# Performance work log

Measured on AMD Instinct MI355X. Metric: run time of the kernel, lower is better.

The kernel has to match this reference:

```python
import jax, jax.numpy as jnp
import numpy as np

D_MODEL = 1024
NUM_HEADS = 16
HEAD_DIM = D_MODEL // NUM_HEADS
SEQ_LEN = 2048
THETA = 10000.0


def setup_inputs() -> dict:
    key = jax.random.key(0)
    ks = jax.random.split(key, 9)
    s = 1.0 / np.sqrt(D_MODEL)
    inp = {
        "x": jax.random.normal(ks[0], (2, SEQ_LEN, D_MODEL), dtype=jnp.float32),
        "Wq": jax.random.uniform(ks[1], (D_MODEL, D_MODEL), jnp.float32, -s, s),
        "bq": jax.random.uniform(ks[2], (D_MODEL,), jnp.float32, -s, s),
        "Wk": jax.random.uniform(ks[3], (D_MODEL, D_MODEL), jnp.float32, -s, s),
        "bk": jax.random.uniform(ks[4], (D_MODEL,), jnp.float32, -s, s),
        "Wv": jax.random.uniform(ks[5], (D_MODEL, D_MODEL), jnp.float32, -s, s),
        "bv": jax.random.uniform(ks[6], (D_MODEL,), jnp.float32, -s, s),
        "Wo": jax.random.uniform(ks[7], (D_MODEL, D_MODEL), jnp.float32, -s, s),
        "bo": jax.random.uniform(ks[8], (D_MODEL,), jnp.float32, -s, s),
    }
    return inp


def _rope_cos_sin(seq_len, dim, theta):
    inv_freq = 1.0 / theta ** (jnp.arange(0, dim, 2, dtype=jnp.float32) / dim)  # [dim/2]
    t = jnp.arange(seq_len, dtype=jnp.float32)
    freqs = jnp.outer(t, inv_freq)  # [S, dim/2]
    return jnp.cos(freqs), jnp.sin(freqs)


def _apply_rope(x, cos, sin):
    # x: [B, H, S, head_dim]; interleaved complex pairs (even, odd)
    x2 = x.reshape(*x.shape[:-1], -1, 2)  # [B,H,S,hd/2,2]
    xe, xo = x2[..., 0], x2[..., 1]
    c = cos[None, None, :, :]
    s = sin[None, None, :, :]
    oe = xe * c - xo * s
    oo = xe * s + xo * c
    return jnp.stack([oe, oo], axis=-1).reshape(x.shape)


def reference(x, Wq, bq, Wk, bk, Wv, bv, Wo, bo):
    B, S, D = x.shape
    H, hd = NUM_HEADS, HEAD_DIM
    q = x @ Wq.T + bq
    k = x @ Wk.T + bk
    v = x @ Wv.T + bv
    # [B, H, S, hd]
    q = q.reshape(B, S, H, hd).transpose(0, 2, 1, 3)
    k = k.reshape(B, S, H, hd).transpose(0, 2, 1, 3)
    v = v.reshape(B, S, H, hd).transpose(0, 2, 1, 3)
    cos, sin = _rope_cos_sin(S, hd, THETA)
    q = _apply_rope(q, cos, sin)
    k = _apply_rope(k, cos, sin)
    scores = jnp.einsum("bhqd,bhkd->bhqk", q, k) / jnp.sqrt(jnp.float32(hd))
    causal = jnp.triu(jnp.ones((S, S), dtype=bool), k=1)
    scores = jnp.where(causal[None, None, :, :], -jnp.inf, scores)
    attn = jax.nn.softmax(scores, axis=-1)
    out = jnp.einsum("bhqk,bhkd->bhqd", attn, v)
    out = out.transpose(0, 2, 1, 3).reshape(B, S, D)
    return out @ Wo.T + bo
```

## Files before the change

kernel.cpp:

```cpp
#include <hip/hip_runtime.h>
#include <hip/hip_bf16.h>

#define S_LEN 2048
#define DM 1024
#define NH 16
#define HD 64
#define M_ROWS 4096
#define LOG2E 1.4426950408889634f

typedef __attribute__((ext_vector_type(8))) short short8;
typedef __attribute__((ext_vector_type(4))) float f32x4;
typedef __attribute__((ext_vector_type(16))) float f32x16;

__device__ inline ushort f2b(float f) {
  union { float f; unsigned u; } v; v.f = f;
  unsigned r = v.u + 0x7fffu + ((v.u >> 16) & 1u);
  return (ushort)(r >> 16);
}

__device__ inline unsigned pk_bf16(float a, float b) {
  __hip_bfloat162 h = __float22bfloat162_rn(make_float2(a, b));
  union { __hip_bfloat162 h; unsigned u; } v; v.h = h;
  return v.u;
}

__device__ inline float fexp2(float x) { return __builtin_amdgcn_exp2f(x); }

__device__ inline void gl_lds16(const void* g, void* l) {
  __builtin_amdgcn_global_load_lds(
      (const __attribute__((address_space(1))) void*)g,
      (__attribute__((address_space(3))) void*)l, 16, 0, 0);
}

__global__ __launch_bounds__(256) void cast_all_kernel(
    const float* __restrict__ x, const float* __restrict__ Wq, const float* __restrict__ Wk,
    const float* __restrict__ Wv, const float* __restrict__ Wo,
    ushort* __restrict__ xb, ushort* __restrict__ Wqb, ushort* __restrict__ Wkb,
    ushort* __restrict__ Wvb, ushort* __restrict__ Wob) {
  int i = blockIdx.x * 256 + threadIdx.x;
  int r = i >> 18, off = i & 0x3FFFF;
  const float4* s;
  uint2* d;
  switch (r) {
    case 0: case 1: case 2: case 3: s = (const float4*)x + i;  d = (uint2*)xb + i;  break;
    case 4: s = (const float4*)Wq + off; d = (uint2*)Wqb + off; break;
    case 5: s = (const float4*)Wk + off; d = (uint2*)Wkb + off; break;
    case 6: s = (const float4*)Wv + off; d = (uint2*)Wvb + off; break;
    default: s = (const float4*)Wo + off; d = (uint2*)Wob + off; break;
  }
  float4 v = *s;
  uint2 o;
  o.x = pk_bf16(v.x, v.y);
  o.y = pk_bf16(v.z, v.w);
  *d = o;
}

__global__ __launch_bounds__(256) void rope_table_kernel(float* __restrict__ C, float* __restrict__ Sn) {
  int idx = blockIdx.x * blockDim.x + threadIdx.x;
  int s = idx >> 5, i = idx & 31;
  float inv = exp2f(-(float)i * (13.287712379549449f / 32.0f));
  float a = (float)s * inv;
  C[idx] = cosf(a);
  Sn[idx] = sinf(a);
}

__device__ inline void gemm128_mainloop(const ushort* __restrict__ A, const ushort* __restrict__ W,
                                        int m0, int n0, f32x4 acc[4][4],
                                        ushort* As, ushort* Bs) {
  const int t = threadIdx.x, lane = t & 63, wave = t >> 6;
  const int wr = (wave >> 1) * 64, wc = (wave & 1) * 64;
  const int lr = lane & 15, lg = lane >> 4;
  const int slot0 = wave * 128 + lane, slot1 = slot0 + 64;
  const int row0 = slot0 >> 2, g0 = (slot0 & 3) ^ (row0 & 3);
  const int row1 = slot1 >> 2, g1 = (slot1 & 3) ^ (row1 & 3);
  const int lo0 = wave * 128 * 8, lo1 = lo0 + 64 * 8;

#pragma unroll
  for (int a = 0; a < 4; a++)
#pragma unroll
    for (int b = 0; b < 4; b++) acc[a][b] = (f32x4){0.f, 0.f, 0.f, 0.f};

  for (int k0 = 0; k0 < DM; k0 += 32) {
    __syncthreads();
    gl_lds16(&A[(size_t)(m0 + row0) * DM + k0 + g0 * 8], &As[lo0]);
    gl_lds16(&A[(size_t)(m0 + row1) * DM + k0 + g1 * 8], &As[lo1]);
    gl_lds16(&W[(size_t)(n0 + row0) * DM + k0 + g0 * 8], &Bs[lo0]);
    gl_lds16(&W[(size_t)(n0 + row1) * DM + k0 + g1 * 8], &Bs[lo1]);
    __syncthreads();
    short8 af[4], bf[4];
#pragma unroll
    for (int mt = 0; mt < 4; mt++)
      af[mt] = *(const short8*)&As[((wr + mt * 16 + lr) * 4 + (lg ^ (lr & 3))) * 8];
#pragma unroll
    for (int nt = 0; nt < 4; nt++)
      bf[nt] = *(const short8*)&Bs[((wc + nt * 16 + lr) * 4 + (lg ^ (lr & 3))) * 8];
#pragma unroll
    for (int mt = 0; mt < 4; mt++)
#pragma unroll
      for (int nt = 0; nt < 4; nt++)
        acc[mt][nt] = __builtin_amdgcn_mfma_f32_16x16x32_bf16(af[mt], bf[nt], acc[mt][nt], 0, 0, 0);
  }
}

__global__ __launch_bounds__(256) void gemm_qkv_kernel(const ushort* __restrict__ xb,
    const ushort* __restrict__ Wqb, const ushort* __restrict__ Wkb, const ushort* __restrict__ Wvb,
    const float* __restrict__ bq, const float* __restrict__ bk, const float* __restrict__ bv,
    const float* __restrict__ ropeC, const float* __restrict__ ropeS,
    ushort* __restrict__ qb, ushort* __restrict__ kb, ushort* __restrict__ vT) {
  __shared__ ushort As[4096];
  __shared__ ushort Bs[4096];
  const int z = blockIdx.z;
  const ushort* W = (z == 0) ? Wqb : ((z == 1) ? Wkb : Wvb);
  const float* bias = (z == 0) ? bq : ((z == 1) ? bk : bv);
  const int m0 = blockIdx.x * 128, n0 = blockIdx.y * 128;
  f32x4 acc[4][4];
  gemm128_mainloop(xb, W, m0, n0, acc, As, Bs);

  const int t = threadIdx.x, lane = t & 63, wave = t >> 6;
  const int wr = (wave >> 1) * 64, wc = (wave & 1) * 64;
  const int lr = lane & 15, lg = lane >> 4;
  const bool evenlane = (lane & 1) == 0;

#pragma unroll
  for (int mt = 0; mt < 4; mt++) {
#pragma unroll
    for (int nt = 0; nt < 4; nt++) {
      const int n = n0 + wc + nt * 16 + lr;
      const float bn = bias[n];
      const int h = n >> 6, d = n & 63, i = (n & 63) >> 1;
#pragma unroll
      for (int r = 0; r < 4; r++) {
        const int m = m0 + wr + mt * 16 + lg * 4 + r;
        const int s = m & (S_LEN - 1);
        const int b = m >> 11;
        float v = acc[mt][nt][r] + bn;
        if (z < 2) {
          float c = ropeC[s * 32 + i];
          float sn = ropeS[s * 32 + i];
          float w = __shfl_xor(v, 1);
          v = v * c + (evenlane ? -w * sn : w * sn);
          if (z == 0) v *= 0.125f;
          ushort* dst = (z == 0) ? qb : kb;
          dst[(((size_t)b * NH + h) * S_LEN + s) * HD + d] = f2b(v);
        } else {
          vT[(((size_t)b * NH + h) * HD + d) * S_LEN + s] = f2b(v);
        }
      }
    }
  }
}

__global__ __launch_bounds__(256) void flash_kernel(const ushort* __restrict__ qb,
                                                    const ushort* __restrict__ kb,
                                                    const ushort* __restrict__ vT,
                                                    ushort* __restrict__ attn_out) {
  __shared__ ushort Ks[2][4096];
  __shared__ ushort VTs[2][4096];
  const int t = threadIdx.x, lane = t & 63, wave = t >> 6;
  const int q31 = lane & 31, h = lane >> 5;
  const int y = blockIdx.y;
  const int qt = (y & 16) ? (int)blockIdx.x : (15 - (int)blockIdx.x);
  const int q0 = qt * 128;
  const int nkt = 2 * qt + 2;
  const ushort* kbh = kb + (size_t)y * S_LEN * HD;
  const ushort* vbh = vT + (size_t)y * HD * S_LEN;

  const int qrow = q0 + wave * 32 + q31;
  const ushort* qptr = qb + ((size_t)y * S_LEN + qrow) * HD + h * 8;
  short8 qf[4];
#pragma unroll
  for (int s = 0; s < 4; s++) qf[s] = *(const short8*)(qptr + s * 16);

  const int slot0 = wave * 128 + lane, slot1 = slot0 + 64;
  const int row0 = slot0 >> 3, g0 = (slot0 & 7) ^ (row0 & 7);
  const int row1 = slot1 >> 3, g1 = (slot1 & 7) ^ (row1 & 7);
  const int lo0 = wave * 128 * 8, lo1 = lo0 + 64 * 8;

  gl_lds16(kbh + (size_t)row0 * HD + g0 * 8, &Ks[0][lo0]);
  gl_lds16(kbh + (size_t)row1 * HD + g1 * 8, &Ks[0][lo1]);
  gl_lds16(vbh + (size_t)row0 * S_LEN + g0 * 8, &VTs[0][lo0]);
  gl_lds16(vbh + (size_t)row1 * S_LEN + g1 * 8, &VTs[0][lo1]);
  __syncthreads();

  f32x16 O[2];
#pragma unroll
  for (int st = 0; st < 2; st++)
#pragma unroll
    for (int r = 0; r < 16; r++) O[st][r] = 0.f;
  float m_i = -1e30f, l_i = 0.f;
  int cur = 0;

  for (int kt = 0; kt < nkt; kt++) {
    if (kt + 1 < nkt) {
      const int k0n = (kt + 1) * 64;
      gl_lds16(kbh + (size_t)(k0n + row0) * HD + g0 * 8, &Ks[cur ^ 1][lo0]);
      gl_lds16(kbh + (size_t)(k0n + row1) * HD + g1 * 8, &Ks[cur ^ 1][lo1]);
      gl_lds16(vbh + (size_t)row0 * S_LEN + k0n + g0 * 8, &VTs[cur ^ 1][lo0]);
      gl_lds16(vbh + (size_t)row1 * S_LEN + k0n + g1 * 8, &VTs[cur ^ 1][lo1]);
    }
    const ushort* Kb = Ks[cur];
    const ushort* Vb = VTs[cur];

    f32x16 sc[2];
#pragma unroll
    for (int st = 0; st < 2; st++)
#pragma unroll
      for (int r = 0; r < 16; r++) sc[st][r] = 0.f;
#pragma unroll
    for (int s = 0; s < 4; s++) {
#pragma unroll
      for (int st = 0; st < 2; st++) {
        const int row = st * 32 + q31;
        const short8 kf = *(const short8*)&Kb[(row * 8 + ((2 * s + h) ^ (row & 7))) * 8];
        sc[st] = __builtin_amdgcn_mfma_f32_32x32x16_bf16(kf, qf[s], sc[st], 0, 0, 0);
      }
    }
    if (kt * 64 + 63 > q0 + wave * 32) {
#pragma unroll
      for (int st = 0; st < 2; st++)
#pragma unroll
        for (int r = 0; r < 16; r++) {
          const int kcol = kt * 64 + st * 32 + (r & 3) + 8 * (r >> 2) + 4 * h;
          if (kcol > qrow) sc[st][r] = -1e30f;
        }
    }
    float mx = sc[0][0];
#pragma unroll
    for (int st = 0; st < 2; st++)
#pragma unroll
      for (int r = 0; r < 16; r++) mx = fmaxf(mx, sc[st][r]);
    mx = fmaxf(mx, __shfl_xor(mx, 32));
    const float mnew = fmaxf(m_i, mx);
    const float alpha = fexp2((m_i - mnew) * LOG2E);
    const float nmw = -mnew * LOG2E;
    float su = 0.f;
#pragma unroll
    for (int st = 0; st < 2; st++)
#pragma unroll
      for (int r = 0; r < 16; r++) {
        const float p = fexp2(fmaf(sc[st][r], LOG2E, nmw));
        sc[st][r] = p;
        su += p;
      }
    su += __shfl_xor(su, 32);
    l_i = l_i * alpha + su;
    m_i = mnew;
#pragma unroll
    for (int st = 0; st < 2; st++)
#pragma unroll
      for (int r = 0; r < 16; r++) O[st][r] *= alpha;

    unsigned pp[8][2];
#pragma unroll
    for (int st = 0; st < 2; st++)
#pragma unroll
      for (int rg = 0; rg < 4; rg++) {
        pp[st * 4 + rg][0] = pk_bf16(sc[st][4 * rg + 0], sc[st][4 * rg + 1]);
        pp[st * 4 + rg][1] = pk_bf16(sc[st][4 * rg + 2], sc[st][4 * rg + 3]);
      }
#pragma unroll
    for (int s = 0; s < 4; s++) {
      const unsigned sA0 = pp[2 * s][0], sA1 = pp[2 * s][1];
      const unsigned sB0 = pp[2 * s + 1][0], sB1 = pp[2 * s + 1][1];
      const unsigned send0 = h ? sA0 : sB0;
      const unsigned send1 = h ? sA1 : sB1;
      const unsigned recv0 = (unsigned)__shfl_xor((int)send0, 32);
      const unsigned recv1 = (unsigned)__shfl_xor((int)send1, 32);
      unsigned bfr[4];
      bfr[0] = h ? recv0 : sA0;
      bfr[1] = h ? recv1 : sA1;
      bfr[2] = h ? sB0 : recv0;
      bfr[3] = h ? sB1 : recv1;
      union { unsigned u[4]; short8 v; } pf;
      pf.u[0] = bfr[0]; pf.u[1] = bfr[1]; pf.u[2] = bfr[2]; pf.u[3] = bfr[3];
#pragma unroll
      for (int st = 0; st < 2; st++) {
        const int row = st * 32 + q31;
        const short8 vf = *(const short8*)&Vb[(row * 8 + ((2 * s + h) ^ (row & 7))) * 8];
        O[st] = __builtin_amdgcn_mfma_f32_32x32x16_bf16(vf, pf.v, O[st], 0, 0, 0);
      }
    }
    __syncthreads();
    cur ^= 1;
  }

  const int b = y >> 4, hh = y & 15;
  const float linv = 1.f / l_i;
  ushort* arow = attn_out + ((size_t)b * S_LEN + qrow) * DM + hh * HD;
#pragma unroll
  for (int st = 0; st < 2; st++)
#pragma unroll
    for (int rg = 0; rg < 4; rg++) {
      const int d0 = st * 32 + 8 * rg + 4 * h;
      *(unsigned*)&arow[d0] = pk_bf16(O[st][4 * rg + 0] * linv, O[st][4 * rg + 1] * linv);
      *(unsigned*)&arow[d0 + 2] = pk_bf16(O[st][4 * rg + 2] * linv, O[st][4 * rg + 3] * linv);
    }
}

__global__ __launch_bounds__(256) void gemm_out_kernel(const ushort* __restrict__ attn,
                                                       const ushort* __restrict__ Wob,
                                                       const float* __restrict__ bo,
                                                       float* __restrict__ out) {
  __shared__ ushort As[4096];
  __shared__ ushort Bs[4096];
  const int m0 = blockIdx.x * 128, n0 = blockIdx.y * 128;
  f32x4 acc[4][4];
  gemm128_mainloop(attn, Wob, m0, n0, acc, As, Bs);

  const int t = threadIdx.x, lane = t & 63, wave = t >> 6;
  const int wr = (wave >> 1) * 64, wc = (wave & 1) * 64;
  const int lr = lane & 15, lg = lane >> 4;
#pragma unroll
  for (int mt = 0; mt < 4; mt++) {
#pragma unroll
    for (int nt = 0; nt < 4; nt++) {
      const int n = n0 + wc + nt * 16 + lr;
      const float bn = bo[n];
#pragma unroll
      for (int r = 0; r < 4; r++) {
        const int m = m0 + wr + mt * 16 + lg * 4 + r;
        out[(size_t)m * DM + n] = acc[mt][nt][r] + bn;
      }
    }
  }
}

extern "C" void kernel_launch(void* const* d_in, const int* in_sizes, int n_in,
                              void* d_out, int out_size, void* d_ws, size_t ws_size,
                              hipStream_t stream) {
  const float* x  = (const float*)d_in[0];
  const float* Wq = (const float*)d_in[1];
  const float* bq = (const float*)d_in[2];
  const float* Wk = (const float*)d_in[3];
  const float* bk = (const float*)d_in[4];
  const float* Wv = (const float*)d_in[5];
  const float* bv = (const float*)d_in[6];
  const float* Wo = (const float*)d_in[7];
  const float* bo = (const float*)d_in[8];
  float* out = (float*)d_out;

  char* ws = (char*)d_ws;
  size_t off = 0;
  auto alloc = [&](size_t bytes) { char* p = ws + off; off += (bytes + 255) & ~255ull; return p; };
  ushort* xb   = (ushort*)alloc((size_t)M_ROWS * DM * 2);
  ushort* Wqb  = (ushort*)alloc((size_t)DM * DM * 2);
  ushort* Wkb  = (ushort*)alloc((size_t)DM * DM * 2);
  ushort* Wvb  = (ushort*)alloc((size_t)DM * DM * 2);
  ushort* Wob  = (ushort*)alloc((size_t)DM * DM * 2);
  ushort* qb   = (ushort*)alloc((size_t)M_ROWS * DM * 2);
  ushort* kb   = (ushort*)alloc((size_t)M_ROWS * DM * 2);
  ushort* vTb  = (ushort*)alloc((size_t)M_ROWS * DM * 2);
  ushort* attn = (ushort*)alloc((size_t)M_ROWS * DM * 2);
  float* ropeC = (float*)alloc((size_t)S_LEN * 32 * 4);
  float* ropeS = (float*)alloc((size_t)S_LEN * 32 * 4);
  (void)ws_size; (void)in_sizes; (void)n_in; (void)out_size;

  cast_all_kernel<<<8192, 256, 0, stream>>>(x, Wq, Wk, Wv, Wo, xb, Wqb, Wkb, Wvb, Wob);
  rope_table_kernel<<<(S_LEN * 32) / 256, 256, 0, stream>>>(ropeC, ropeS);
  gemm_qkv_kernel<<<dim3(M_ROWS / 128, DM / 128, 3), 256, 0, stream>>>(
      xb, Wqb, Wkb, Wvb, bq, bk, bv, ropeC, ropeS, qb, kb, vTb);
  flash_kernel<<<dim3(16, 2 * NH), 256, 0, stream>>>(qb, kb, vTb, attn);
  gemm_out_kernel<<<dim3(M_ROWS / 128, DM / 128), 256, 0, stream>>>(attn, Wob, bo, out);
}
```

Baseline: 215.4 us.

## Split flash attention across KV halves, restage QKV epilogue, retile output GEMM

Flash attention now splits each (batch, head) KV range into even and odd 64-key tiles, processed by separate blocks. This doubles the grid. A new combine kernel merges the two partial outputs using their per-row max and sum. The QKV GEMM moves to a 64-wide K step and stages its output tile through LDS, so RoPE is applied in a vectorized pass and Q, K and V^T are written with coalesced 16-byte stores. The output GEMM uses 128x64 tiles to launch more blocks. The cost is an extra kernel launch, a round trip of partial outputs through memory, and a finite mask value that must stay harmless for fully masked half-tiles.

```diff
diff --git a/kernel.cpp b/kernel.cpp
--- a/kernel.cpp
+++ b/kernel.cpp
@@ -7,6 +7,7 @@
 #define HD 64
 #define M_ROWS 4096
 #define LOG2E 1.4426950408889634f
+#define MASKVAL -1.0e4f
 
 typedef __attribute__((ext_vector_type(8))) short short8;
 typedef __attribute__((ext_vector_type(4))) float f32x4;
@@ -16,6 +17,10 @@
   union { float f; unsigned u; } v; v.f = f;
   unsigned r = v.u + 0x7fffu + ((v.u >> 16) & 1u);
   return (ushort)(r >> 16);
+}
+
+__device__ inline float b2f(ushort u) {
+  union { unsigned u; float f; } v; v.u = ((unsigned)u) << 16; return v.f;
 }
 
 __device__ inline unsigned pk_bf16(float a, float b) {
@@ -64,88 +69,128 @@
   Sn[idx] = sinf(a);
 }
 
-__device__ inline void gemm128_mainloop(const ushort* __restrict__ A, const ushort* __restrict__ W,
-                                        int m0, int n0, f32x4 acc[4][4],
-                                        ushort* As, ushort* Bs) {
-  const int t = threadIdx.x, lane = t & 63, wave = t >> 6;
-  const int wr = (wave >> 1) * 64, wc = (wave & 1) * 64;
-  const int lr = lane & 15, lg = lane >> 4;
-  const int slot0 = wave * 128 + lane, slot1 = slot0 + 64;
-  const int row0 = slot0 >> 2, g0 = (slot0 & 3) ^ (row0 & 3);
-  const int row1 = slot1 >> 2, g1 = (slot1 & 3) ^ (row1 & 3);
-  const int lo0 = wave * 128 * 8, lo1 = lo0 + 64 * 8;
-
-#pragma unroll
-  for (int a = 0; a < 4; a++)
-#pragma unroll
-    for (int b = 0; b < 4; b++) acc[a][b] = (f32x4){0.f, 0.f, 0.f, 0.f};
-
-  for (int k0 = 0; k0 < DM; k0 += 32) {
-    __syncthreads();
-    gl_lds16(&A[(size_t)(m0 + row0) * DM + k0 + g0 * 8], &As[lo0]);
-    gl_lds16(&A[(size_t)(m0 + row1) * DM + k0 + g1 * 8], &As[lo1]);
-    gl_lds16(&W[(size_t)(n0 + row0) * DM + k0 + g0 * 8], &Bs[lo0]);
-    gl_lds16(&W[(size_t)(n0 + row1) * DM + k0 + g1 * 8], &Bs[lo1]);
-    __syncthreads();
-    short8 af[4], bf[4];
-#pragma unroll
-    for (int mt = 0; mt < 4; mt++)
-      af[mt] = *(const short8*)&As[((wr + mt * 16 + lr) * 4 + (lg ^ (lr & 3))) * 8];
-#pragma unroll
-    for (int nt = 0; nt < 4; nt++)
-      bf[nt] = *(const short8*)&Bs[((wc + nt * 16 + lr) * 4 + (lg ^ (lr & 3))) * 8];
-#pragma unroll
-    for (int mt = 0; mt < 4; mt++)
-#pragma unroll
-      for (int nt = 0; nt < 4; nt++)
-        acc[mt][nt] = __builtin_amdgcn_mfma_f32_16x16x32_bf16(af[mt], bf[nt], acc[mt][nt], 0, 0, 0);
-  }
-}
-
 __global__ __launch_bounds__(256) void gemm_qkv_kernel(const ushort* __restrict__ xb,
     const ushort* __restrict__ Wqb, const ushort* __restrict__ Wkb, const ushort* __restrict__ Wvb,
     const float* __restrict__ bq, const float* __restrict__ bk, const float* __restrict__ bv,
     const float* __restrict__ ropeC, const float* __restrict__ ropeS,
     ushort* __restrict__ qb, ushort* __restrict__ kb, ushort* __restrict__ vT) {
-  __shared__ ushort As[4096];
-  __shared__ ushort Bs[4096];
+  __shared__ ushort lds[128 * 136];
+  ushort* As = lds;
+  ushort* Bs = lds + 8192;
   const int z = blockIdx.z;
   const ushort* W = (z == 0) ? Wqb : ((z == 1) ? Wkb : Wvb);
   const float* bias = (z == 0) ? bq : ((z == 1) ? bk : bv);
   const int m0 = blockIdx.x * 128, n0 = blockIdx.y * 128;
-  f32x4 acc[4][4];
-  gemm128_mainloop(xb, W, m0, n0, acc, As, Bs);
-
   const int t = threadIdx.x, lane = t & 63, wave = t >> 6;
   const int wr = (wave >> 1) * 64, wc = (wave & 1) * 64;
   const int lr = lane & 15, lg = lane >> 4;
-  const bool evenlane = (lane & 1) == 0;
-
+
+  int rows_[4], gs_[4], slots_[4];
+#pragma unroll
+  for (int j = 0; j < 4; j++) {
+    const int slot = wave * 256 + j * 64 + lane;
+    slots_[j] = slot;
+    rows_[j] = slot >> 3;
+    gs_[j] = (slot & 7) ^ (rows_[j] & 7);
+  }
+
+  f32x4 acc[4][4];
+#pragma unroll
+  for (int a = 0; a < 4; a++)
+#pragma unroll
+    for (int b = 0; b < 4; b++) acc[a][b] = (f32x4){0.f, 0.f, 0.f, 0.f};
+
+  for (int k0 = 0; k0 < DM; k0 += 64) {
+    __syncthreads();
+#pragma unroll
+    for (int j = 0; j < 4; j++)
+      gl_lds16(&xb[(size_t)(m0 + rows_[j]) * DM + k0 + gs_[j] * 8], &As[slots_[j] * 8]);
+#pragma unroll
+    for (int j = 0; j < 4; j++)
+      gl_lds16(&W[(size_t)(n0 + rows_[j]) * DM + k0 + gs_[j] * 8], &Bs[slots_[j] * 8]);
+    __syncthreads();
+#pragma unroll
+    for (int s32 = 0; s32 < 2; s32++) {
+      short8 af[4], bf[4];
+#pragma unroll
+      for (int mt = 0; mt < 4; mt++) {
+        const int row = wr + mt * 16 + lr;
+        af[mt] = *(const short8*)&As[(row * 8 + ((s32 * 4 + lg) ^ (row & 7))) * 8];
+      }
+#pragma unroll
+      for (int nt = 0; nt < 4; nt++) {
+        const int row = wc + nt * 16 + lr;
+        bf[nt] = *(const short8*)&Bs[(row * 8 + ((s32 * 4 + lg) ^ (row & 7))) * 8];
+      }
+#pragma unroll
+      for (int mt = 0; mt < 4; mt++)
+#pragma unroll
+        for (int nt = 0; nt < 4; nt++)
+          acc[mt][nt] = __builtin_amdgcn_mfma_f32_16x16x32_bf16(af[mt], bf[nt], acc[mt][nt], 0, 0, 0);
+    }
+  }
+
+  __syncthreads();
 #pragma unroll
   for (int mt = 0; mt < 4; mt++) {
 #pragma unroll
     for (int nt = 0; nt < 4; nt++) {
-      const int n = n0 + wc + nt * 16 + lr;
-      const float bn = bias[n];
-      const int h = n >> 6, d = n & 63, i = (n & 63) >> 1;
+      const int nloc = wc + nt * 16 + lr;
+      const float bn = bias[n0 + nloc];
 #pragma unroll
       for (int r = 0; r < 4; r++) {
-        const int m = m0 + wr + mt * 16 + lg * 4 + r;
-        const int s = m & (S_LEN - 1);
-        const int b = m >> 11;
-        float v = acc[mt][nt][r] + bn;
-        if (z < 2) {
-          float c = ropeC[s * 32 + i];
-          float sn = ropeS[s * 32 + i];
-          float w = __shfl_xor(v, 1);
-          v = v * c + (evenlane ? -w * sn : w * sn);
-          if (z == 0) v *= 0.125f;
-          ushort* dst = (z == 0) ? qb : kb;
-          dst[(((size_t)b * NH + h) * S_LEN + s) * HD + d] = f2b(v);
-        } else {
-          vT[(((size_t)b * NH + h) * HD + d) * S_LEN + s] = f2b(v);
-        }
-      }
+        const int mloc = wr + mt * 16 + lg * 4 + r;
+        const ushort v = f2b(acc[mt][nt][r] + bn);
+        if (z < 2) lds[mloc * 136 + nloc] = v;
+        else       lds[nloc * 136 + mloc] = v;
+      }
+    }
+  }
+  __syncthreads();
+
+  const int b = m0 >> 11;
+  if (z < 2) {
+    ushort* dst = (z == 0) ? qb : kb;
+    const float qscale = (z == 0) ? 0.125f : 1.0f;
+#pragma unroll
+    for (int c = 0; c < 8; c++) {
+      const int sloc = c * 16 + (t >> 4);
+      const int nloc = (t & 15) * 8;
+      short8 val = *(const short8*)&lds[sloc * 136 + nloc];
+      const int s = (m0 + sloc) & (S_LEN - 1);
+      const int h = (n0 + nloc) >> 6;
+      const int d0 = nloc & 63;
+      const float4 cv = *(const float4*)&ropeC[s * 32 + d0 / 2];
+      const float4 sv = *(const float4*)&ropeS[s * 32 + d0 / 2];
+      uint4 o;
+      {
+        float e = b2f((ushort)val[0]), od = b2f((ushort)val[1]);
+        o.x = pk_bf16((e * cv.x - od * sv.x) * qscale, (e * sv.x + od * cv.x) * qscale);
+      }
+      {
+        float e = b2f((ushort)val[2]), od = b2f((ushort)val[3]);
+        o.y = pk_bf16((e * cv.y - od * sv.y) * qscale, (e * sv.y + od * cv.y) * qscale);
+      }
+      {
+        float e = b2f((ushort)val[4]), od = b2f((ushort)val[5]);
+        o.z = pk_bf16((e * cv.z - od * sv.z) * qscale, (e * sv.z + od * cv.z) * qscale);
+      }
+      {
+        float e = b2f((ushort)val[6]), od = b2f((ushort)val[7]);
+        o.w = pk_bf16((e * cv.w - od * sv.w) * qscale, (e * sv.w + od * cv.w) * qscale);
+      }
+      *(uint4*)&dst[(((size_t)b * NH + h) * S_LEN + s) * HD + d0] = o;
+    }
+  } else {
+    const int sbase = m0 & (S_LEN - 1);
+#pragma unroll
+    for (int c = 0; c < 8; c++) {
+      const int nloc = c * 16 + (t >> 4);
+      const int s0 = (t & 15) * 8;
+      short8 val = *(const short8*)&lds[nloc * 136 + s0];
+      const int h = (n0 + nloc) >> 6;
+      const int d = nloc & 63;
+      *(short8*)&vT[(((size_t)b * NH + h) * HD + d) * S_LEN + sbase + s0] = val;
     }
   }
 }
@@ -153,20 +198,21 @@
 __global__ __launch_bounds__(256) void flash_kernel(const ushort* __restrict__ qb,
                                                     const ushort* __restrict__ kb,
                                                     const ushort* __restrict__ vT,
-                                                    ushort* __restrict__ attn_out) {
+                                                    ushort* __restrict__ Oh,
+                                                    float2* __restrict__ ml) {
   __shared__ ushort Ks[2][4096];
   __shared__ ushort VTs[2][4096];
   const int t = threadIdx.x, lane = t & 63, wave = t >> 6;
   const int q31 = lane & 31, h = lane >> 5;
   const int y = blockIdx.y;
+  const int bh = y >> 1, half = y & 1;
   const int qt = (y & 16) ? (int)blockIdx.x : (15 - (int)blockIdx.x);
   const int q0 = qt * 128;
-  const int nkt = 2 * qt + 2;
-  const ushort* kbh = kb + (size_t)y * S_LEN * HD;
-  const ushort* vbh = vT + (size_t)y * HD * S_LEN;
+  const ushort* kbh = kb + (size_t)bh * S_LEN * HD;
+  const ushort* vbh = vT + (size_t)bh * HD * S_LEN;
 
   const int qrow = q0 + wave * 32 + q31;
-  const ushort* qptr = qb + ((size_t)y * S_LEN + qrow) * HD + h * 8;
+  const ushort* qptr = qb + ((size_t)bh * S_LEN + qrow) * HD + h * 8;
   short8 qf[4];
 #pragma unroll
   for (int s = 0; s < 4; s++) qf[s] = *(const short8*)(qptr + s * 16);
@@ -176,10 +222,13 @@
   const int row1 = slot1 >> 3, g1 = (slot1 & 7) ^ (row1 & 7);
   const int lo0 = wave * 128 * 8, lo1 = lo0 + 64 * 8;
 
-  gl_lds16(kbh + (size_t)row0 * HD + g0 * 8, &Ks[0][lo0]);
-  gl_lds16(kbh + (size_t)row1 * HD + g1 * 8, &Ks[0][lo1]);
-  gl_lds16(vbh + (size_t)row0 * S_LEN + g0 * 8, &VTs[0][lo0]);
-  gl_lds16(vbh + (size_t)row1 * S_LEN + g1 * 8, &VTs[0][lo1]);
+  {
+    const int k00 = half * 64;
+    gl_lds16(kbh + (size_t)(k00 + row0) * HD + g0 * 8, &Ks[0][lo0]);
+    gl_lds16(kbh + (size_t)(k00 + row1) * HD + g1 * 8, &Ks[0][lo1]);
+    gl_lds16(vbh + (size_t)row0 * S_LEN + k00 + g0 * 8, &VTs[0][lo0]);
+    gl_lds16(vbh + (size_t)row1 * S_LEN + k00 + g1 * 8, &VTs[0][lo1]);
+  }
   __syncthreads();
 
   f32x16 O[2];
@@ -187,12 +236,13 @@
   for (int st = 0; st < 2; st++)
 #pragma unroll
     for (int r = 0; r < 16; r++) O[st][r] = 0.f;
-  float m_i = -1e30f, l_i = 0.f;
+  float m_i = MASKVAL, l_i = 0.f;
   int cur = 0;
 
-  for (int kt = 0; kt < nkt; kt++) {
-    if (kt + 1 < nkt) {
-      const int k0n = (kt + 1) * 64;
+  for (int idx = 0; idx <= qt; idx++) {
+    const int kt = half + 2 * idx;
+    if (idx < qt) {
+      const int k0n = (kt + 2) * 64;
       gl_lds16(kbh + (size_t)(k0n + row0) * HD + g0 * 8, &Ks[cur ^ 1][lo0]);
       gl_lds16(kbh + (size_t)(k0n + row1) * HD + g1 * 8, &Ks[cur ^ 1][lo1]);
       gl_lds16(vbh + (size_t)row0 * S_LEN + k0n + g0 * 8, &VTs[cur ^ 1][lo0]);
@@ -221,7 +271,7 @@
 #pragma unroll
         for (int r = 0; r < 16; r++) {
           const int kcol = kt * 64 + st * 32 + (r & 3) + 8 * (r >> 2) + 4 * h;
-          if (kcol > qrow) sc[st][r] = -1e30f;
+          if (kcol > qrow) sc[st][r] = MASKVAL;
         }
     }
     float mx = sc[0][0];
@@ -266,13 +316,11 @@
       const unsigned send1 = h ? sA1 : sB1;
       const unsigned recv0 = (unsigned)__shfl_xor((int)send0, 32);
       const unsigned recv1 = (unsigned)__shfl_xor((int)send1, 32);
-      unsigned bfr[4];
-      bfr[0] = h ? recv0 : sA0;
-      bfr[1] = h ? recv1 : sA1;
-      bfr[2] = h ? sB0 : recv0;
-      bfr[3] = h ? sB1 : recv1;
       union { unsigned u[4]; short8 v; } pf;
-      pf.u[0] = bfr[0]; pf.u[1] = bfr[1]; pf.u[2] = bfr[2]; pf.u[3] = bfr[3];
+      pf.u[0] = h ? recv0 : sA0;
+      pf.u[1] = h ? recv1 : sA1;
+      pf.u[2] = h ? sB0 : recv0;
+      pf.u[3] = h ? sB1 : recv1;
 #pragma unroll
       for (int st = 0; st < 2; st++) {
         const int row = st * 32 + q31;
@@ -284,17 +332,47 @@
     cur ^= 1;
   }
 
-  const int b = y >> 4, hh = y & 15;
-  const float linv = 1.f / l_i;
-  ushort* arow = attn_out + ((size_t)b * S_LEN + qrow) * DM + hh * HD;
+  ushort* obase = Oh + (((size_t)half * 32 + bh) * S_LEN + qrow) * HD;
 #pragma unroll
   for (int st = 0; st < 2; st++)
 #pragma unroll
     for (int rg = 0; rg < 4; rg++) {
       const int d0 = st * 32 + 8 * rg + 4 * h;
-      *(unsigned*)&arow[d0] = pk_bf16(O[st][4 * rg + 0] * linv, O[st][4 * rg + 1] * linv);
-      *(unsigned*)&arow[d0 + 2] = pk_bf16(O[st][4 * rg + 2] * linv, O[st][4 * rg + 3] * linv);
-    }
+      uint2 w;
+      w.x = pk_bf16(O[st][4 * rg + 0], O[st][4 * rg + 1]);
+      w.y = pk_bf16(O[st][4 * rg + 2], O[st][4 * rg + 3]);
+      *(uint2*)&obase[d0] = w;
+    }
+  if (h == 0) ml[((size_t)half * 32 + bh) * S_LEN + qrow] = make_float2(m_i, l_i);
+}
+
+__global__ __launch_bounds__(256) void combine_kernel(const ushort* __restrict__ Oh,
+                                                      const float2* __restrict__ ml,
+                                                      ushort* __restrict__ attn) {
+  const int tid = blockIdx.x * 256 + threadIdx.x;
+  const int d8 = tid & 7;
+  const int q = (tid >> 3) & (S_LEN - 1);
+  const int bh = tid >> 14;
+  const float2 ml0 = ml[(size_t)bh * S_LEN + q];
+  const float2 ml1 = ml[((size_t)32 + bh) * S_LEN + q];
+  const float m = fmaxf(ml0.x, ml1.x);
+  const float w0 = fexp2((ml0.x - m) * LOG2E);
+  const float w1 = fexp2((ml1.x - m) * LOG2E);
+  const float inv = 1.f / (ml0.y * w0 + ml1.y * w1);
+  const uint4 a = *(const uint4*)&Oh[((size_t)bh * S_LEN + q) * HD + d8 * 8];
+  const uint4 bb = *(const uint4*)&Oh[(((size_t)32 + bh) * S_LEN + q) * HD + d8 * 8];
+  const unsigned au[4] = {a.x, a.y, a.z, a.w};
+  const unsigned bu[4] = {bb.x, bb.y, bb.z, bb.w};
+  uint4 o;
+  unsigned* op = (unsigned*)&o;
+#pragma unroll
+  for (int j = 0; j < 4; j++) {
+    const float a0 = b2f((ushort)(au[j] & 0xffff)), a1 = b2f((ushort)(au[j] >> 16));
+    const float b0 = b2f((ushort)(bu[j] & 0xffff)), b1 = b2f((ushort)(bu[j] >> 16));
+    op[j] = pk_bf16((a0 * w0 + b0 * w1) * inv, (a1 * w0 + b1 * w1) * inv);
+  }
+  const int b = bh >> 4, hh = bh & 15;
+  *(uint4*)&attn[((size_t)b * S_LEN + q) * DM + hh * HD + d8 * 8] = o;
 }
 
 __global__ __launch_bounds__(256) void gemm_out_kernel(const ushort* __restrict__ attn,
@@ -302,23 +380,56 @@
                                                        const float* __restrict__ bo,
                                                        float* __restrict__ out) {
   __shared__ ushort As[4096];
-  __shared__ ushort Bs[4096];
-  const int m0 = blockIdx.x * 128, n0 = blockIdx.y * 128;
-  f32x4 acc[4][4];
-  gemm128_mainloop(attn, Wob, m0, n0, acc, As, Bs);
-
+  __shared__ ushort Bs[2048];
+  const int m0 = blockIdx.x * 128, n0 = blockIdx.y * 64;
   const int t = threadIdx.x, lane = t & 63, wave = t >> 6;
-  const int wr = (wave >> 1) * 64, wc = (wave & 1) * 64;
+  const int wm = (wave >> 1) * 64, wn = (wave & 1) * 32;
   const int lr = lane & 15, lg = lane >> 4;
+  const int slotA0 = wave * 128 + lane, slotA1 = slotA0 + 64;
+  const int rowA0 = slotA0 >> 2, gA0 = (slotA0 & 3) ^ (rowA0 & 3);
+  const int rowA1 = slotA1 >> 2, gA1 = (slotA1 & 3) ^ (rowA1 & 3);
+  const int slotB = wave * 64 + lane;
+  const int rowB = slotB >> 2, gB = (slotB & 3) ^ (rowB & 3);
+
+  f32x4 acc[4][2];
+#pragma unroll
+  for (int a = 0; a < 4; a++)
+#pragma unroll
+    for (int b = 0; b < 2; b++) acc[a][b] = (f32x4){0.f, 0.f, 0.f, 0.f};
+
+  for (int k0 = 0; k0 < DM; k0 += 32) {
+    __syncthreads();
+    gl_lds16(&attn[(size_t)(m0 + rowA0) * DM + k0 + gA0 * 8], &As[slotA0 * 8]);
+    gl_lds16(&attn[(size_t)(m0 + rowA1) * DM + k0 + gA1 * 8], &As[slotA1 * 8]);
+    gl_lds16(&Wob[(size_t)(n0 + rowB) * DM + k0 + gB * 8], &Bs[slotB * 8]);
+    __syncthreads();
+    short8 af[4], bf[2];
+#pragma unroll
+    for (int mt = 0; mt < 4; mt++) {
+      const int row = wm + mt * 16 + lr;
+      af[mt] = *(const short8*)&As[(row * 4 + (lg ^ (row & 3))) * 8];
+    }
+#pragma unroll
+    for (int nt = 0; nt < 2; nt++) {
+      const int row = wn + nt * 16 + lr;
+      bf[nt] = *(const short8*)&Bs[(row * 4 + (lg ^ (row & 3))) * 8];
+    }
+#pragma unroll
+    for (int mt = 0; mt < 4; mt++)
+#pragma unroll
+      for (int nt = 0; nt < 2; nt++)
+        acc[mt][nt] = __builtin_amdgcn_mfma_f32_16x16x32_bf16(af[mt], bf[nt], acc[mt][nt], 0, 0, 0);
+  }
+
 #pragma unroll
   for (int mt = 0; mt < 4; mt++) {
 #pragma unroll
-    for (int nt = 0; nt < 4; nt++) {
-      const int n = n0 + wc + nt * 16 + lr;
+    for (int nt = 0; nt < 2; nt++) {
+      const int n = n0 + wn + nt * 16 + lr;
       const float bn = bo[n];
 #pragma unroll
       for (int r = 0; r < 4; r++) {
-        const int m = m0 + wr + mt * 16 + lg * 4 + r;
+        const int m = m0 + wm + mt * 16 + lg * 4 + r;
         out[(size_t)m * DM + n] = acc[mt][nt][r] + bn;
       }
     }
@@ -351,6 +462,8 @@
   ushort* kb   = (ushort*)alloc((size_t)M_ROWS * DM * 2);
   ushort* vTb  = (ushort*)alloc((size_t)M_ROWS * DM * 2);
   ushort* attn = (ushort*)alloc((size_t)M_ROWS * DM * 2);
+  ushort* Ohb  = (ushort*)alloc((size_t)2 * 32 * S_LEN * HD * 2);
+  float2* mlb  = (float2*)alloc((size_t)2 * 32 * S_LEN * 8);
   float* ropeC = (float*)alloc((size_t)S_LEN * 32 * 4);
   float* ropeS = (float*)alloc((size_t)S_LEN * 32 * 4);
   (void)ws_size; (void)in_sizes; (void)n_in; (void)out_size;
@@ -359,6 +472,7 @@
   rope_table_kernel<<<(S_LEN * 32) / 256, 256, 0, stream>>>(ropeC, ropeS);
   gemm_qkv_kernel<<<dim3(M_ROWS / 128, DM / 128, 3), 256, 0, stream>>>(
       xb, Wqb, Wkb, Wvb, bq, bk, bv, ropeC, ropeS, qb, kb, vTb);
-  flash_kernel<<<dim3(16, 2 * NH), 256, 0, stream>>>(qb, kb, vTb, attn);
-  gemm_out_kernel<<<dim3(M_ROWS / 128, DM / 128), 256, 0, stream>>>(attn, Wob, bo, out);
-}
+  flash_kernel<<<dim3(16, 64), 256, 0, stream>>>(qb, kb, vTb, Ohb, mlb);
+  combine_kernel<<<2048, 256, 0, stream>>>(Ohb, mlb, attn);
+  gemm_out_kernel<<<dim3(M_ROWS / 128, DM / 64), 256, 0, stream>>>(attn, Wob, bo, out);
+}
```

Result: no change. 212.1 us (-1.6%).
